# Optimization experiments

Hardware: AMD Instinct MI355X
Metric: run time of the kernel (lower is better)

The kernel has to match this reference:

```python
import jax, jax.numpy as jnp
import numpy as np

B, S, F = 4096, 128, 8
H1, H2 = 64, 32


def setup_inputs() -> dict:
    key = jax.random.key(0)
    ks = jax.random.split(key, 12)
    rn = lambda k, shape, scale: jax.random.normal(k, shape, dtype=jnp.float32) * scale
    return {
        "x": rn(ks[0], (B, S, F), 1.0),
        "time": jax.random.uniform(ks[1], (B, 1), dtype=jnp.float32),
        # linear_combine: (S*F + 1) -> S*F
        "W_combine": rn(ks[2], (S * F, S * F + 1), 1.0 / np.sqrt(S * F + 1)),
        "b_combine": jnp.zeros((S * F,), jnp.float32),
        # LSTM layer 1 (bias=False), gate order i,f,g,o like torch
        "W_ih1": rn(ks[3], (4 * H1, F), 1.0 / np.sqrt(H1)),
        "W_hh1": rn(ks[4], (4 * H1, H1), 1.0 / np.sqrt(H1)),
        # LSTM layer 2 (bias=True)
        "W_ih2": rn(ks[5], (4 * H2, H1), 1.0 / np.sqrt(H2)),
        "W_hh2": rn(ks[6], (4 * H2, H2), 1.0 / np.sqrt(H2)),
        "b_ih2": rn(ks[7], (4 * H2,), 0.05),
        "b_hh2": rn(ks[8], (4 * H2,), 0.05),
        # l_linear_supervised: (H2*S) -> 1
        "W_out": rn(ks[9], (1, H2 * S), 1.0 / np.sqrt(H2 * S)),
        "b_out": jnp.zeros((1,), jnp.float32),
    }


def _lstm(x, W_ih, W_hh, b):
    """batch_first LSTM, zero initial state. x: [B,S,D] -> hidden seq [B,S,H]."""
    Bq = x.shape[0]
    H = W_hh.shape[1]
    # precompute input contribution for all timesteps: [B,S,4H]
    xg = jnp.einsum('bsd,gd->bsg', x, W_ih) + b

    def step(carry, xg_t):
        h, c = carry
        g = xg_t + h @ W_hh.T
        i, f, gg, o = jnp.split(g, 4, axis=-1)  # torch gate order i,f,g,o
        c = jax.nn.sigmoid(f) * c + jax.nn.sigmoid(i) * jnp.tanh(gg)
        h = jax.nn.sigmoid(o) * jnp.tanh(c)
        return (h, c), h

    h0 = jnp.zeros((Bq, H), x.dtype)
    (_, _), hs = jax.lax.scan(step, (h0, h0), jnp.swapaxes(xg, 0, 1))
    return jnp.swapaxes(hs, 0, 1)


def reference(x, time, W_combine, b_combine, W_ih1, W_hh1, W_ih2, W_hh2,
              b_ih2, b_hh2, W_out, b_out):
    Bq = x.shape[0]
    # future_time_as_input == 1 branch: flatten, append time, linear + relu
    xf = jnp.concatenate([x.reshape(Bq, -1), time.reshape(Bq, -1)], axis=1)
    xf = jax.nn.relu(xf @ W_combine.T + b_combine)
    x1 = xf.reshape(Bq, S, F)
    h1 = _lstm(x1, W_ih1, W_hh1, jnp.zeros((4 * H1,), x.dtype))  # [B,S,64]
    h2 = _lstm(h1, W_ih2, W_hh2, b_ih2 + b_hh2)                   # [B,S,32]
    return h2.reshape(Bq, -1) @ W_out.T + b_out                   # [B,1]
```

## Files before the change

### kernel.cpp

```cpp
#include <hip/hip_runtime.h>
#include <math.h>


typedef _Float16 f16x8 __attribute__((ext_vector_type(8)));
typedef float f32x4 __attribute__((ext_vector_type(4)));

union H8 { uint4 q; _Float16 h[8]; f16x8 v; };
union H2u { unsigned u; _Float16 h[2]; };

#define MF(A, B, C) __builtin_amdgcn_mfma_f32_16x16x32_f16(A, B, C, 0, 0, 0)

__device__ __forceinline__ float sigm(float x) {
  return __builtin_amdgcn_rcpf(1.f + __builtin_amdgcn_exp2f(x * -1.44269504f));
}
__device__ __forceinline__ float tanh_fast(float x) {
  return 1.f - 2.f * __builtin_amdgcn_rcpf(1.f + __builtin_amdgcn_exp2f(x * 2.88539008f));
}

#define CROW 72

__global__ __launch_bounds__(256, 2) void combine_mfma(
    const float* __restrict__ x, const float* __restrict__ tme,
    const float* __restrict__ Wc, const float* __restrict__ bc,
    unsigned* __restrict__ x1u)
{
  __shared__ __align__(16) _Float16 sA[128][CROW];
  __shared__ __align__(16) _Float16 sB[64][CROW];
  __shared__ float sT[128];
  __shared__ float sWl[64];
  __shared__ float sBc[64];
  _Float16 (*Cst)[CROW] = sA;

  const int tid = threadIdx.x;
  const int lane = tid & 63;
  const int w = tid >> 6;
  const int r = lane & 15, grp = lane >> 4;
  const int M0 = blockIdx.y * 128, N0 = blockIdx.x * 64;

  if (tid < 128) sT[tid] = tme[M0 + tid];
  else if (tid < 192) sWl[tid - 128] = Wc[(size_t)(N0 + tid - 128) * 1025 + 1024];
  else sBc[tid - 192] = bc[N0 + tid - 192];

  f32x4 acc[2][4];
#pragma unroll
  for (int i = 0; i < 2; ++i)
#pragma unroll
    for (int j = 0; j < 4; ++j) acc[i][j] = f32x4{0.f, 0.f, 0.f, 0.f};

  for (int kt = 0; kt < 1024; kt += 64) {
#pragma unroll
    for (int i = 0; i < 8; ++i) {
      int idx = tid + i * 256;
      int row = idx >> 4, kq = idx & 15;
      float4 v = *(const float4*)&x[(size_t)(M0 + row) * 1024 + kt + kq * 4];
      H2u p0, p1;
      p0.h[0] = (_Float16)v.x; p0.h[1] = (_Float16)v.y;
      p1.h[0] = (_Float16)v.z; p1.h[1] = (_Float16)v.w;
      *(uint2*)&sA[row][kq * 4] = uint2{p0.u, p1.u};
    }
#pragma unroll
    for (int i = 0; i < 4; ++i) {
      int idx = tid + i * 256;
      int row = idx >> 4, kq = idx & 15;
      float4 v = *(const float4*)&Wc[(size_t)(N0 + row) * 1025 + kt + kq * 4];
      H2u p0, p1;
      p0.h[0] = (_Float16)v.x; p0.h[1] = (_Float16)v.y;
      p1.h[0] = (_Float16)v.z; p1.h[1] = (_Float16)v.w;
      *(uint2*)&sB[row][kq * 4] = uint2{p0.u, p1.u};
    }
    __syncthreads();

    H8 af[2][2], bf[4][2];
#pragma unroll
    for (int i = 0; i < 2; ++i)
#pragma unroll
      for (int c = 0; c < 2; ++c)
        af[i][c].q = *(const uint4*)&sA[w * 32 + i * 16 + r][c * 32 + grp * 8];
#pragma unroll
    for (int j = 0; j < 4; ++j)
#pragma unroll
      for (int c = 0; c < 2; ++c)
        bf[j][c].q = *(const uint4*)&sB[j * 16 + r][c * 32 + grp * 8];
#pragma unroll
    for (int i = 0; i < 2; ++i)
#pragma unroll
      for (int j = 0; j < 4; ++j) {
        acc[i][j] = MF(af[i][0].v, bf[j][0].v, acc[i][j]);
        acc[i][j] = MF(af[i][1].v, bf[j][1].v, acc[i][j]);
      }
    __syncthreads();
  }

#pragma unroll
  for (int i = 0; i < 2; ++i) {
#pragma unroll
    for (int j = 0; j < 4; ++j) {
      int n = j * 16 + r;
      float wl = sWl[n], bv = sBc[n];
#pragma unroll
      for (int q = 0; q < 4; ++q) {
        int mm = w * 32 + i * 16 + 4 * grp + q;
        float v = acc[i][j][q] + sT[mm] * wl + bv;
        Cst[mm][n] = (_Float16)fmaxf(v, 0.f);
      }
    }
  }
  __syncthreads();
#pragma unroll
  for (int i = 0; i < 4; ++i) {
    int idx = tid + i * 256;
    int row = idx >> 3, c8 = idx & 7;
    uint4 v = *(const uint4*)&Cst[row][c8 * 8];
    *(uint4*)&x1u[(size_t)(M0 + row) * 512 + (N0 >> 1) + c8 * 4] = v;
  }
}

#define ROW1 72
#define ROW2 40

__global__ __launch_bounds__(768, 3) void lstm_fused_mfma(
    const unsigned* __restrict__ x1u,
    const float* __restrict__ Wih1, const float* __restrict__ Whh1,
    const float* __restrict__ Wih2, const float* __restrict__ Whh2,
    const float* __restrict__ bih2, const float* __restrict__ bhh2,
    const float* __restrict__ Wout, const float* __restrict__ bout,
    float* __restrict__ out)
{
  __shared__ __align__(16) unsigned sxw[128 * 16 * 4];
  __shared__ float sWoT[32 * 132];
  __shared__ __align__(16) unsigned short sh1[2][16][ROW1];
  __shared__ __align__(16) unsigned short sh2[2][16][ROW2];
  __shared__ float sOut[8][16];

  const int tid = threadIdx.x;
  const int lane = tid & 63;
  const int w = tid >> 6;
  const int col = lane & 15;
  const int grp = lane >> 4;
  const int b0 = blockIdx.x * 16;
  const bool loWave = (w < 8);
  const int p0 = loWave ? w : (8 + 2 * (w - 8));

  const int m1 = col >> 2, g1 = col & 3;
  f16x8 A1[2][3];
#pragma unroll
  for (int jj = 0; jj < 2; ++jj) {
    const int p = loWave ? p0 : (p0 + jj);
    const int wr = g1 * 64 + 4 * p + m1;
#pragma unroll
    for (int c = 0; c < 3; ++c) {
      H8 f;
#pragma unroll
      for (int q = 0; q < 8; ++q) {
        float wv = 0.f;
        if (c < 2) wv = Whh1[wr * 64 + c * 32 + grp * 8 + q];
        else if (grp == 0) wv = Wih1[wr * 8 + q];
        f.h[q] = (_Float16)wv;
      }
      A1[jj][c] = f.v;
    }
  }
  f16x8 A2[3];
  float bias2[4] = {0.f, 0.f, 0.f, 0.f};
  const int h2o = 4 * (w & 7) + grp;
  if (loWave) {
    const int wr = g1 * 32 + 4 * w + m1;
#pragma unroll
    for (int c = 0; c < 3; ++c) {
      H8 f;
#pragma unroll
      for (int q = 0; q < 8; ++q) {
        float wv = (c < 2) ? Wih2[wr * 64 + c * 32 + grp * 8 + q]
                           : Whh2[wr * 32 + grp * 8 + q];
        f.h[q] = (_Float16)wv;
      }
      A2[c] = f.v;
    }
#pragma unroll
    for (int r = 0; r < 4; ++r)
      bias2[r] = bih2[r * 32 + h2o] + bhh2[r * 32 + h2o];
  }

  for (int idx = tid; idx < 4096; idx += 768) {
    int t = idx >> 5, h = idx & 31;
    sWoT[h * 132 + t] = Wout[idx];
  }
  {
    unsigned short* z = &sh1[0][0][0];
    for (int i2 = tid; i2 < 2 * 16 * ROW1; i2 += 768) z[i2] = 0;
    unsigned short* z2 = &sh2[0][0][0];
    for (int i2 = tid; i2 < 2 * 16 * ROW2; i2 += 768) z2[i2] = 0;
  }
  for (int idx = tid; idx < 16 * 512; idx += 768) {
    int bb = idx >> 9, rem = idx & 511;
    int t = rem >> 2, pr = rem & 3;
    sxw[t * 64 + bb * 4 + pr] = x1u[(size_t)(b0 + bb) * 512 + rem];
  }
  __syncthreads();

  float c1a = 0.f, c1b = 0.f, c2 = 0.f, accO = 0.f, wov = 0.f;
  H8 sxv;
  sxv.q = *(const uint4*)&sxw[col * 4];

#define PHASE(T, CUR, DO_L1, DO_L2)                                            \
  {                                                                            \
    H8 s0, s1;                                                                 \
    s0.q = *(const uint4*)&sh1[CUR][col][grp * 8];                             \
    s1.q = *(const uint4*)&sh1[CUR][col][32 + grp * 8];                        \
    H8 sxn;                                                                    \
    { const int tn = ((T) < 127) ? (T) + 1 : 127;                              \
      sxn.q = *(const uint4*)&sxw[tn * 64 + col * 4]; }                        \
    if (loWave) {                                                              \
      const float won = sWoT[h2o * 132 + (((T) < 127) ? (T) : 127)];           \
      if (DO_L2) {                                                             \
        H8 s2;                                                                 \
        s2.q = *(const uint4*)&sh2[CUR][col][grp * 8];                         \
        f32x4 a = {bias2[0], bias2[1], bias2[2], bias2[3]};                    \
        a = MF(A2[0], s0.v, a);                                                \
        a = MF(A2[1], s1.v, a);                                                \
        a = MF(A2[2], s2.v, a);                                                \
        float ig = sigm(a[0]), fg = sigm(a[1]);                                \
        float tg = tanh_fast(a[2]), og = sigm(a[3]);                           \
        float cc = fg * c2 + ig * tg;                                          \
        c2 = cc;                                                               \
        float hn = og * tanh_fast(cc);                                         \
        accO += hn * wov;                                                      \
        *(_Float16*)&sh2[(CUR) ^ 1][col][h2o] = (_Float16)hn;                  \
      }                                                                        \
      if (DO_L1) {                                                             \
        f32x4 a = {0.f, 0.f, 0.f, 0.f};                                        \
        a = MF(A1[0][0], s0.v, a);                                             \
        a = MF(A1[0][1], s1.v, a);                                             \
        a = MF(A1[0][2], sxv.v, a);                                            \
        float ig = sigm(a[0]), fg = sigm(a[1]);                                \
        float tg = tanh_fast(a[2]), og = sigm(a[3]);                           \
        float cc = fg * c1a + ig * tg;                                         \
        c1a = cc;                                                              \
        *(_Float16*)&sh1[(CUR) ^ 1][col][4 * p0 + grp] =                       \
            (_Float16)(og * tanh_fast(cc));                                    \
      }                                                                        \
      wov = won;                                                               \
    } else if (DO_L1) {                                                        \
      f32x4 aA = {0.f, 0.f, 0.f, 0.f}, aB = {0.f, 0.f, 0.f, 0.f};              \
      aA = MF(A1[0][0], s0.v, aA);                                             \
      aB = MF(A1[1][0], s0.v, aB);                                             \
      aA = MF(A1[0][1], s1.v, aA);                                             \
      aB = MF(A1[1][1], s1.v, aB);                                             \
      aA = MF(A1[0][2], sxv.v, aA);                                            \
      aB = MF(A1[1][2], sxv.v, aB);                                            \
      float ig0 = sigm(aA[0]), fg0 = sigm(aA[1]);                              \
      float tg0 = tanh_fast(aA[2]), og0 = sigm(aA[3]);                         \
      float cc0 = fg0 * c1a + ig0 * tg0;                                       \
      c1a = cc0;                                                               \
      *(_Float16*)&sh1[(CUR) ^ 1][col][4 * p0 + grp] =                         \
          (_Float16)(og0 * tanh_fast(cc0));                                    \
      float ig1 = sigm(aB[0]), fg1 = sigm(aB[1]);                              \
      float tg1 = tanh_fast(aB[2]), og1 = sigm(aB[3]);                         \
      float cc1 = fg1 * c1b + ig1 * tg1;                                       \
      c1b = cc1;                                                               \
      *(_Float16*)&sh1[(CUR) ^ 1][col][4 * (p0 + 1) + grp] =                   \
          (_Float16)(og1 * tanh_fast(cc1));                                    \
    }                                                                          \
    sxv = sxn;                                                                 \
    __syncthreads();                                                           \
  }

  PHASE(0, 0, true, false);
  PHASE(1, 1, true, true);
  for (int tt = 1; tt < 64; ++tt) {
    const int t0 = 2 * tt;
    PHASE(t0, 0, true, true);
    PHASE(t0 + 1, 1, true, true);
  }
  PHASE(128, 0, false, true);
#undef PHASE

  if (loWave) {
    accO += __shfl_xor(accO, 16);
    accO += __shfl_xor(accO, 32);
    if (grp == 0) sOut[w][col] = accO;
  }
  __syncthreads();
  if (tid < 16) {
    float s = bout[0];
#pragma unroll
    for (int q = 0; q < 8; ++q) s += sOut[q][tid];
    out[b0 + tid] = s;
  }
}

extern "C" void kernel_launch(void* const* d_in, const int* in_sizes, int n_in,
                              void* d_out, int out_size, void* d_ws, size_t ws_size,
                              hipStream_t stream) {
  const float* x    = (const float*)d_in[0];
  const float* tme  = (const float*)d_in[1];
  const float* Wc   = (const float*)d_in[2];
  const float* bc   = (const float*)d_in[3];
  const float* Wih1 = (const float*)d_in[4];
  const float* Whh1 = (const float*)d_in[5];
  const float* Wih2 = (const float*)d_in[6];
  const float* Whh2 = (const float*)d_in[7];
  const float* bih2 = (const float*)d_in[8];
  const float* bhh2 = (const float*)d_in[9];
  const float* Wout = (const float*)d_in[10];
  const float* bout = (const float*)d_in[11];
  float* outp = (float*)d_out;
  unsigned* x1u = (unsigned*)d_ws;

  dim3 gA(16, 32);
  combine_mfma<<<gA, 256, 0, stream>>>(x, tme, Wc, bc, x1u);
  lstm_fused_mfma<<<256, 768, 0, stream>>>(x1u, Wih1, Whh1, Wih2, Whh2,
                                           bih2, bhh2, Wout, bout, outp);
}
```

Before: 116.4 us.

## Rebalance fused LSTM across 8 uniform waves and fold log2e into weights

```diff
diff --git a/kernel.cpp b/kernel.cpp
--- a/kernel.cpp
+++ b/kernel.cpp
@@ -6,15 +6,21 @@
 typedef float f32x4 __attribute__((ext_vector_type(4)));
 
 union H8 { uint4 q; _Float16 h[8]; f16x8 v; };
-union H2u { unsigned u; _Float16 h[2]; };
 
 #define MF(A, B, C) __builtin_amdgcn_mfma_f32_16x16x32_f16(A, B, C, 0, 0, 0)
-
-__device__ __forceinline__ float sigm(float x) {
-  return __builtin_amdgcn_rcpf(1.f + __builtin_amdgcn_exp2f(x * -1.44269504f));
-}
-__device__ __forceinline__ float tanh_fast(float x) {
-  return 1.f - 2.f * __builtin_amdgcn_rcpf(1.f + __builtin_amdgcn_exp2f(x * 2.88539008f));
+#define LOG2E 1.44269504f
+
+__device__ __forceinline__ float sigm_pre(float y) {
+  return __builtin_amdgcn_rcpf(1.f + __builtin_amdgcn_exp2f(-y));
+}
+__device__ __forceinline__ float tanh_pre(float y) {
+  return 1.f - 2.f * __builtin_amdgcn_rcpf(1.f + __builtin_amdgcn_exp2f(y + y));
+}
+__device__ __forceinline__ float tanh_raw(float c) {
+  return 1.f - 2.f * __builtin_amdgcn_rcpf(1.f + __builtin_amdgcn_exp2f(c * 2.88539008f));
+}
+__device__ __forceinline__ unsigned pkrtz(float a, float b) {
+  return __builtin_bit_cast(unsigned, __builtin_amdgcn_cvt_pkrtz(a, b));
 }
 
 #define CROW 72
@@ -53,20 +59,14 @@
       int idx = tid + i * 256;
       int row = idx >> 4, kq = idx & 15;
       float4 v = *(const float4*)&x[(size_t)(M0 + row) * 1024 + kt + kq * 4];
-      H2u p0, p1;
-      p0.h[0] = (_Float16)v.x; p0.h[1] = (_Float16)v.y;
-      p1.h[0] = (_Float16)v.z; p1.h[1] = (_Float16)v.w;
-      *(uint2*)&sA[row][kq * 4] = uint2{p0.u, p1.u};
+      *(uint2*)&sA[row][kq * 4] = uint2{pkrtz(v.x, v.y), pkrtz(v.z, v.w)};
     }
 #pragma unroll
     for (int i = 0; i < 4; ++i) {
       int idx = tid + i * 256;
       int row = idx >> 4, kq = idx & 15;
       float4 v = *(const float4*)&Wc[(size_t)(N0 + row) * 1025 + kt + kq * 4];
-      H2u p0, p1;
-      p0.h[0] = (_Float16)v.x; p0.h[1] = (_Float16)v.y;
-      p1.h[0] = (_Float16)v.z; p1.h[1] = (_Float16)v.w;
-      *(uint2*)&sB[row][kq * 4] = uint2{p0.u, p1.u};
+      *(uint2*)&sB[row][kq * 4] = uint2{pkrtz(v.x, v.y), pkrtz(v.z, v.w)};
     }
     __syncthreads();
 
@@ -118,7 +118,7 @@
 #define ROW1 72
 #define ROW2 40
 
-__global__ __launch_bounds__(768, 3) void lstm_fused_mfma(
+__global__ __launch_bounds__(512, 2) void lstm_fused_mfma(
     const unsigned* __restrict__ x1u,
     const float* __restrict__ Wih1, const float* __restrict__ Whh1,
     const float* __restrict__ Wih2, const float* __restrict__ Whh2,
@@ -135,36 +135,36 @@
   const int tid = threadIdx.x;
   const int lane = tid & 63;
   const int w = tid >> 6;
+  const int vw = w >> 1;
+  const int wsub = w & 1;
   const int col = lane & 15;
   const int grp = lane >> 4;
   const int b0 = blockIdx.x * 16;
-  const bool loWave = (w < 8);
-  const int p0 = loWave ? w : (8 + 2 * (w - 8));
 
   const int m1 = col >> 2, g1 = col & 3;
-  f16x8 A1[2][3];
+  f16x8 A1h[2][2];
+  f16x8 A1x[2];
 #pragma unroll
   for (int jj = 0; jj < 2; ++jj) {
-    const int p = loWave ? p0 : (p0 + jj);
-    const int wr = g1 * 64 + 4 * p + m1;
-#pragma unroll
-    for (int c = 0; c < 3; ++c) {
+    const int wr = g1 * 64 + vw * 16 + 4 * m1 + (2 * wsub + jj);
+#pragma unroll
+    for (int c = 0; c < 2; ++c) {
       H8 f;
 #pragma unroll
-      for (int q = 0; q < 8; ++q) {
-        float wv = 0.f;
-        if (c < 2) wv = Whh1[wr * 64 + c * 32 + grp * 8 + q];
-        else if (grp == 0) wv = Wih1[wr * 8 + q];
-        f.h[q] = (_Float16)wv;
-      }
-      A1[jj][c] = f.v;
-    }
+      for (int q = 0; q < 8; ++q)
+        f.h[q] = (_Float16)(Whh1[wr * 64 + c * 32 + grp * 8 + q] * LOG2E);
+      A1h[jj][c] = f.v;
+    }
+    H8 fx;
+#pragma unroll
+    for (int q = 0; q < 8; ++q)
+      fx.h[q] = (grp == 0) ? (_Float16)(Wih1[wr * 8 + q] * LOG2E) : (_Float16)0.f;
+    A1x[jj] = fx.v;
   }
   f16x8 A2[3];
-  float bias2[4] = {0.f, 0.f, 0.f, 0.f};
-  const int h2o = 4 * (w & 7) + grp;
-  if (loWave) {
-    const int wr = g1 * 32 + 4 * w + m1;
+  const int u = 2 * vw + wsub;
+  {
+    const int wr = g1 * 32 + 4 * u + m1;
 #pragma unroll
     for (int c = 0; c < 3; ++c) {
       H8 f;
@@ -172,96 +172,78 @@
       for (int q = 0; q < 8; ++q) {
         float wv = (c < 2) ? Wih2[wr * 64 + c * 32 + grp * 8 + q]
                            : Whh2[wr * 32 + grp * 8 + q];
-        f.h[q] = (_Float16)wv;
+        f.h[q] = (_Float16)(wv * LOG2E);
       }
       A2[c] = f.v;
     }
-#pragma unroll
-    for (int r = 0; r < 4; ++r)
-      bias2[r] = bih2[r * 32 + h2o] + bhh2[r * 32 + h2o];
-  }
-
-  for (int idx = tid; idx < 4096; idx += 768) {
+  }
+  const int h2o = 4 * u + grp;
+  f32x4 b2q;
+#pragma unroll
+  for (int r = 0; r < 4; ++r)
+    b2q[r] = (bih2[r * 32 + h2o] + bhh2[r * 32 + h2o]) * LOG2E;
+  const f32x4 zq = {0.f, 0.f, 0.f, 0.f};
+
+  for (int idx = tid; idx < 4096; idx += 512) {
     int t = idx >> 5, h = idx & 31;
     sWoT[h * 132 + t] = Wout[idx];
   }
   {
     unsigned short* z = &sh1[0][0][0];
-    for (int i2 = tid; i2 < 2 * 16 * ROW1; i2 += 768) z[i2] = 0;
+    for (int i2 = tid; i2 < 2 * 16 * ROW1; i2 += 512) z[i2] = 0;
     unsigned short* z2 = &sh2[0][0][0];
-    for (int i2 = tid; i2 < 2 * 16 * ROW2; i2 += 768) z2[i2] = 0;
-  }
-  for (int idx = tid; idx < 16 * 512; idx += 768) {
+    for (int i2 = tid; i2 < 2 * 16 * ROW2; i2 += 512) z2[i2] = 0;
+  }
+  for (int idx = tid; idx < 16 * 512; idx += 512) {
     int bb = idx >> 9, rem = idx & 511;
     int t = rem >> 2, pr = rem & 3;
     sxw[t * 64 + bb * 4 + pr] = x1u[(size_t)(b0 + bb) * 512 + rem];
   }
   __syncthreads();
 
-  float c1a = 0.f, c1b = 0.f, c2 = 0.f, accO = 0.f, wov = 0.f;
-  H8 sxv;
-  sxv.q = *(const uint4*)&sxw[col * 4];
+  float c1a = 0.f, c1b = 0.f, c2 = 0.f, accO = 0.f;
 
 #define PHASE(T, CUR, DO_L1, DO_L2)                                            \
   {                                                                            \
-    H8 s0, s1;                                                                 \
+    H8 s0, s1, s2;                                                             \
     s0.q = *(const uint4*)&sh1[CUR][col][grp * 8];                             \
     s1.q = *(const uint4*)&sh1[CUR][col][32 + grp * 8];                        \
-    H8 sxn;                                                                    \
-    { const int tn = ((T) < 127) ? (T) + 1 : 127;                              \
-      sxn.q = *(const uint4*)&sxw[tn * 64 + col * 4]; }                        \
-    if (loWave) {                                                              \
-      const float won = sWoT[h2o * 132 + (((T) < 127) ? (T) : 127)];           \
-      if (DO_L2) {                                                             \
-        H8 s2;                                                                 \
-        s2.q = *(const uint4*)&sh2[CUR][col][grp * 8];                         \
-        f32x4 a = {bias2[0], bias2[1], bias2[2], bias2[3]};                    \
-        a = MF(A2[0], s0.v, a);                                                \
-        a = MF(A2[1], s1.v, a);                                                \
-        a = MF(A2[2], s2.v, a);                                                \
-        float ig = sigm(a[0]), fg = sigm(a[1]);                                \
-        float tg = tanh_fast(a[2]), og = sigm(a[3]);                           \
-        float cc = fg * c2 + ig * tg;                                          \
-        c2 = cc;                                                               \
-        float hn = og * tanh_fast(cc);                                         \
-        accO += hn * wov;                                                      \
-        *(_Float16*)&sh2[(CUR) ^ 1][col][h2o] = (_Float16)hn;                  \
-      }                                                                        \
-      if (DO_L1) {                                                             \
-        f32x4 a = {0.f, 0.f, 0.f, 0.f};                                        \
-        a = MF(A1[0][0], s0.v, a);                                             \
-        a = MF(A1[0][1], s1.v, a);                                             \
-        a = MF(A1[0][2], sxv.v, a);                                            \
-        float ig = sigm(a[0]), fg = sigm(a[1]);                                \
-        float tg = tanh_fast(a[2]), og = sigm(a[3]);                           \
-        float cc = fg * c1a + ig * tg;                                         \
-        c1a = cc;                                                              \
-        *(_Float16*)&sh1[(CUR) ^ 1][col][4 * p0 + grp] =                       \
-            (_Float16)(og * tanh_fast(cc));                                    \
-      }                                                                        \
-      wov = won;                                                               \
-    } else if (DO_L1) {                                                        \
-      f32x4 aA = {0.f, 0.f, 0.f, 0.f}, aB = {0.f, 0.f, 0.f, 0.f};              \
-      aA = MF(A1[0][0], s0.v, aA);                                             \
-      aB = MF(A1[1][0], s0.v, aB);                                             \
-      aA = MF(A1[0][1], s1.v, aA);                                             \
-      aB = MF(A1[1][1], s1.v, aB);                                             \
-      aA = MF(A1[0][2], sxv.v, aA);                                            \
-      aB = MF(A1[1][2], sxv.v, aB);                                            \
-      float ig0 = sigm(aA[0]), fg0 = sigm(aA[1]);                              \
-      float tg0 = tanh_fast(aA[2]), og0 = sigm(aA[3]);                         \
+    s2.q = *(const uint4*)&sh2[CUR][col][grp * 8];                             \
+    if (DO_L2) {                                                               \
+      const float won = sWoT[h2o * 132 + (T) - 1];                             \
+      f32x4 a = MF(A2[2], s2.v, b2q);                                          \
+      a = MF(A2[0], s0.v, a);                                                  \
+      a = MF(A2[1], s1.v, a);                                                  \
+      float ig = sigm_pre(a[0]), fg = sigm_pre(a[1]);                          \
+      float tg = tanh_pre(a[2]), og = sigm_pre(a[3]);                          \
+      float cc = fg * c2 + ig * tg;                                            \
+      c2 = cc;                                                                 \
+      float hn = og * tanh_raw(cc);                                            \
+      accO = fmaf(hn, won, accO);                                              \
+      *(_Float16*)&sh2[(CUR) ^ 1][col][h2o] = (_Float16)hn;                    \
+    }                                                                          \
+    if (DO_L1) {                                                               \
+      H8 sx;                                                                   \
+      sx.q = *(const uint4*)&sxw[(T) * 64 + col * 4];                          \
+      f32x4 a0 = MF(A1x[0], sx.v, zq);                                         \
+      f32x4 a1 = MF(A1x[1], sx.v, zq);                                         \
+      a0 = MF(A1h[0][0], s0.v, a0);                                            \
+      a1 = MF(A1h[1][0], s0.v, a1);                                            \
+      a0 = MF(A1h[0][1], s1.v, a0);                                            \
+      a1 = MF(A1h[1][1], s1.v, a1);                                            \
+      float ig0 = sigm_pre(a0[0]), fg0 = sigm_pre(a0[1]);                      \
+      float tg0 = tanh_pre(a0[2]), og0 = sigm_pre(a0[3]);                      \
       float cc0 = fg0 * c1a + ig0 * tg0;                                       \
       c1a = cc0;                                                               \
-      *(_Float16*)&sh1[(CUR) ^ 1][col][4 * p0 + grp] =                         \
-          (_Float16)(og0 * tanh_fast(cc0));                                    \
-      float ig1 = sigm(aB[0]), fg1 = sigm(aB[1]);                              \
-      float tg1 = tanh_fast(aB[2]), og1 = sigm(aB[3]);                         \
+      float h0 = og0 * tanh_raw(cc0);                                          \
+      float ig1 = sigm_pre(a1[0]), fg1 = sigm_pre(a1[1]);                      \
+      float tg1 = tanh_pre(a1[2]), og1 = sigm_pre(a1[3]);                      \
       float cc1 = fg1 * c1b + ig1 * tg1;                                       \
       c1b = cc1;                                                               \
-      *(_Float16*)&sh1[(CUR) ^ 1][col][4 * (p0 + 1) + grp] =                   \
-          (_Float16)(og1 * tanh_fast(cc1));                                    \
+      float h1v = og1 * tanh_raw(cc1);                                         \
+      *(unsigned*)&sh1[(CUR) ^ 1][col][vw * 16 + 4 * grp + 2 * wsub] =         \
+          pkrtz(h0, h1v);                                                      \
     }                                                                          \
-    sxv = sxn;                                                                 \
     __syncthreads();                                                           \
   }
 
@@ -275,11 +257,9 @@
   PHASE(128, 0, false, true);
 #undef PHASE
 
-  if (loWave) {
-    accO += __shfl_xor(accO, 16);
-    accO += __shfl_xor(accO, 32);
-    if (grp == 0) sOut[w][col] = accO;
-  }
+  accO += __shfl_xor(accO, 16);
+  accO += __shfl_xor(accO, 32);
+  if (grp == 0) sOut[u][col] = accO;
   __syncthreads();
   if (tid < 16) {
     float s = bout[0];
@@ -309,6 +289,6 @@
 
   dim3 gA(16, 32);
   combine_mfma<<<gA, 256, 0, stream>>>(x, tme, Wc, bc, x1u);
-  lstm_fused_mfma<<<256, 768, 0, stream>>>(x1u, Wih1, Whh1, Wih2, Whh2,
+  lstm_fused_mfma<<<256, 512, 0, stream>>>(x1u, Wih1, Whh1, Wih2, Whh2,
                                            bih2, bhh2, Wout, bout, outp);
 }
```

New measurement: 105.7 us. 9.2% less time.
